# Optimization experiments

Hardware: AMD Instinct MI355X
Metric: run time of the kernel (lower is better)

Reference implementation:

```python
import jax, jax.numpy as jnp
import numpy as np

N = 6144       # nodes
E = 12288      # edges (~2N for a sparse simplicial complex)
NF = 32        # node features
EF = 16        # edge features
NH = [32, 32]  # node_hidden
EH = [16, 16]  # edge_hidden
EPS = 1e-5


def setup_inputs() -> dict:
    key = jax.random.key(0)
    ks = jax.random.split(key, 24)
    s = 0.1  # weight init scale
    inp = {}
    inp["X_n"] = jax.random.normal(ks[0], (N, NF), jnp.float32)
    inp["X_e"] = jax.random.normal(ks[1], (E, EF), jnp.float32)
    # normalized adjacency-like operator (non-negative, row mass ~1)
    inp["A_tilde"] = jax.random.uniform(ks[2], (N, N), jnp.float32) * (1.0 / N)
    # normalized Hodge-1 Laplacian-like operator
    inp["L1_tilde"] = jax.random.normal(ks[3], (E, E), jnp.float32) * (1.0 / np.sqrt(E))
    # incidence-like operator
    inp["B1"] = jax.random.normal(ks[4], (N, E), jnp.float32) * (1.0 / np.sqrt(E))
    # GNN linear layers: weight [out, in] (torch convention)
    inp["gnn_W0"] = jax.random.normal(ks[5], (NH[0], NF), jnp.float32) * s
    inp["gnn_b0"] = jnp.zeros((NH[0],), jnp.float32)
    inp["gnn_W1"] = jax.random.normal(ks[6], (NH[1], NH[0]), jnp.float32) * s
    inp["gnn_b1"] = jnp.zeros((NH[1],), jnp.float32)
    # HoSC layer 0: theta in=EF out=EH[0], BN params
    inp["th_W0"] = jax.random.normal(ks[7], (EH[0], EF), jnp.float32) * s
    inp["th_b0"] = jnp.zeros((EH[0],), jnp.float32)
    inp["bn_g0"] = jnp.ones((EH[0],), jnp.float32)
    inp["bn_b0"] = jnp.zeros((EH[0],), jnp.float32)
    # HoSC layer 1: input collapses to 1 channel (max keepdim)
    inp["th_W1"] = jax.random.normal(ks[8], (EH[1], 1), jnp.float32) * s
    inp["th_b1"] = jnp.zeros((EH[1],), jnp.float32)
    inp["bn_g1"] = jnp.ones((EH[1],), jnp.float32)
    inp["bn_b1"] = jnp.zeros((EH[1],), jnp.float32)
    # head: fc1 in = NH[-1] + len(EH) = 34, out = 2N; fc2 out = 1
    inp["fc1_W"] = jax.random.normal(ks[9], (2 * N, NH[-1] + len(EH)), jnp.float32) * s
    inp["fc1_b"] = jnp.zeros((2 * N,), jnp.float32)
    inp["fc2_W"] = jax.random.normal(ks[10], (1, 2 * N), jnp.float32) * s
    inp["fc2_b"] = jnp.zeros((1,), jnp.float32)
    return inp


def _gnn_layer(A, H, W, b):
    # H <- relu((A @ H) @ W^T + b)
    return jax.nn.relu(jnp.matmul(jnp.matmul(A, H), W.T) + b)


def _hosc_layer(Z, L1, W, b, g, beta):
    Zt = jnp.matmul(Z, W.T) + b            # theta
    Zc = jnp.matmul(L1, Zt)                # Laplacian conv
    m = jnp.mean(Zc, axis=0)               # BatchNorm1d (training-mode batch stats)
    v = jnp.var(Zc, axis=0)
    Zp = jax.nn.relu(g * (Zc - m) * jax.lax.rsqrt(v + EPS) + beta)
    return jnp.max(Zp, axis=1, keepdims=True)  # [E, 1]


def reference(X_n, X_e, A_tilde, L1_tilde, B1,
              gnn_W0, gnn_b0, gnn_W1, gnn_b1,
              th_W0, th_b0, bn_g0, bn_b0,
              th_W1, th_b1, bn_g1, bn_b1,
              fc1_W, fc1_b, fc2_W, fc2_b):
    # GNN over nodes
    H = _gnn_layer(A_tilde, X_n, gnn_W0, gnn_b0)
    H_n = _gnn_layer(A_tilde, H, gnn_W1, gnn_b1)      # [N, NH[-1]]
    # HoSC over edges
    Z0 = _hosc_layer(X_e, L1_tilde, th_W0, th_b0, bn_g0, bn_b0)  # [E, 1]
    Z1 = _hosc_layer(Z0, L1_tilde, th_W1, th_b1, bn_g1, bn_b1)   # [E, 1]
    Z_cat = jnp.concatenate([Z0, Z1], axis=1)         # [E, 2]
    H_e = jnp.matmul(B1, Z_cat)                       # [N, 2]
    # head
    Hcat = jnp.concatenate([H_n, H_e], axis=1)        # [N, 34]
    f = jax.nn.relu(jnp.matmul(Hcat, fc1_W.T) + fc1_b)
    f = jnp.matmul(f, fc2_W.T) + fc2_b                # [N, 1]
    return jax.nn.sigmoid(f).squeeze(-1)              # [N]
```

## Files before the change

### kernel.cpp

```cpp
#include <hip/hip_runtime.h>
#include <hip/hip_bf16.h>
#include <math.h>

#define NND 6144
#define NED 12288
static constexpr float EPS_BN = 1e-5f;

#define HN_OFF    0
#define HE_OFF    196608
#define ST_OFF    208896
#define Y_OFF     208960
#define T0_OFF    405568
#define T1_OFF    602176
#define Z0_OFF    798784
#define Z1_OFF    811072
#define U_OFF     823360
#define S_OFF     835648
#define PP_OFF    847936

typedef float floatx4 __attribute__((ext_vector_type(4)));

__device__ __forceinline__ float4 ntload4(const float* p) {
  floatx4 v = __builtin_nontemporal_load(reinterpret_cast<const floatx4*>(p));
  return make_float4(v.x, v.y, v.z, v.w);
}
__device__ __forceinline__ float4 ld4(const float* p) {
  return *reinterpret_cast<const float4*>(p);
}

__global__ void init_ws(float* __restrict__ p, int n) {
  int i = blockIdx.x * blockDim.x + threadIdx.x;
  if (i < n) p[i] = 0.f;
}

template<int IC, int OC>
__global__ void small_mm_T(const float* __restrict__ X, const float* __restrict__ W,
                           const float* __restrict__ bias, float* __restrict__ CT, int M) {
  int m = blockIdx.x * blockDim.x + threadIdx.x;
  if (m >= M) return;
  float x[IC];
  #pragma unroll
  for (int k = 0; k < IC; k += 4) {
    float4 v = ld4(X + (size_t)m * IC + k);
    x[k] = v.x; x[k+1] = v.y; x[k+2] = v.z; x[k+3] = v.w;
  }
  #pragma unroll
  for (int oc = 0; oc < OC; ++oc) {
    float s = bias ? bias[oc] : 0.f;
    #pragma unroll
    for (int k = 0; k < IC; ++k) s = fmaf(x[k], W[oc * IC + k], s);
    CT[(size_t)oc * M + m] = s;
  }
}

template<int NC, int CG, bool RELU, bool STATS, bool NT>
__global__ __launch_bounds__(256, 3)
void gemm_lds(const float* __restrict__ A, const float* __restrict__ YT,
              const float* __restrict__ bias, float* __restrict__ out,
              float* __restrict__ stats, int K) {
  constexpr int RG = 4 / CG;
  constexpr int ROWS = RG * 4;
  constexpr int SF4 = NC / 4;
  __shared__ float Yb[NC][256];
  __shared__ float sst[32];

  const int tid = threadIdx.x;
  const int lane = tid & 63;
  const int w = tid >> 6;
  const int cg = w % CG, rg = w / CG;
  const int r0 = blockIdx.x * ROWS + rg * 4;
  const int c0 = cg * 16;

  const float* ap[4];
  #pragma unroll
  for (int r = 0; r < 4; ++r) ap[r] = A + (size_t)(r0 + r) * K;

  int srow[SF4], scol[SF4];
  #pragma unroll
  for (int i = 0; i < SF4; ++i) {
    int f = tid + 256 * i;
    srow[i] = f >> 6;
    scol[i] = (f & 63) * 4;
  }

  float4 sreg[SF4], av[4], av2[4];
  float acc[4][16];
  #pragma unroll
  for (int r = 0; r < 4; ++r)
    #pragma unroll
    for (int c = 0; c < 16; ++c) acc[r][c] = 0.f;

  auto stage = [&](int kb) {
    #pragma unroll
    for (int i = 0; i < SF4; ++i)
      sreg[i] = ld4(YT + (size_t)srow[i] * K + kb + scol[i]);
  };
  auto loadA = [&](int kb, float4* dst) {
    #pragma unroll
    for (int r = 0; r < 4; ++r)
      dst[r] = NT ? ntload4(ap[r] + kb + lane * 4) : ld4(ap[r] + kb + lane * 4);
  };

  stage(0);
  loadA(0, av2);

  for (int kb = 0; kb < K; kb += 256) {
    __syncthreads();
    #pragma unroll
    for (int i = 0; i < SF4; ++i)
      *reinterpret_cast<float4*>(&Yb[srow[i]][scol[i]]) = sreg[i];
    #pragma unroll
    for (int r = 0; r < 4; ++r) av[r] = av2[r];
    if (kb + 256 < K) {
      stage(kb + 256);
      loadA(kb + 256, av2);
    }
    __syncthreads();
    #pragma unroll
    for (int c = 0; c < 16; ++c) {
      const float4 y = *reinterpret_cast<const float4*>(&Yb[c0 + c][lane * 4]);
      #pragma unroll
      for (int r = 0; r < 4; ++r) {
        acc[r][c] = fmaf(av[r].x, y.x, acc[r][c]);
        acc[r][c] = fmaf(av[r].y, y.y, acc[r][c]);
        acc[r][c] = fmaf(av[r].z, y.z, acc[r][c]);
        acc[r][c] = fmaf(av[r].w, y.w, acc[r][c]);
      }
    }
  }

  float wv[64];
  #pragma unroll
  for (int r = 0; r < 4; ++r)
    #pragma unroll
    for (int c = 0; c < 16; ++c) wv[r * 16 + c] = acc[r][c];
  #pragma unroll
  for (int b = 5; b >= 0; --b) {
    const int m = 1 << b;
    const bool hi = (lane & m) != 0;
    #pragma unroll
    for (int i = 0; i < (1 << b); ++i) {
      float a  = wv[i];
      float bb = wv[i + (1 << b)];
      float send = hi ? a : bb;
      float recv = __shfl_xor(send, m, 64);
      wv[i] = (hi ? bb : a) + recv;
    }
  }

  const int rsel = lane >> 4, csel = lane & 15;
  float v = wv[0] + (bias ? bias[c0 + csel] : 0.f);
  if (RELU) v = fmaxf(v, 0.f);
  out[(size_t)(r0 + rsel) * NC + c0 + csel] = v;

  if (STATS) {
    if (tid < 32) sst[tid] = 0.f;
    __syncthreads();
    float sv = v, qv = v * v;
    sv += __shfl_xor(sv, 16, 64); sv += __shfl_xor(sv, 32, 64);
    qv += __shfl_xor(qv, 16, 64); qv += __shfl_xor(qv, 32, 64);
    if (lane < 16) { atomicAdd(&sst[csel], sv); atomicAdd(&sst[16 + csel], qv); }
    __syncthreads();
    if (tid < 32) atomicAdd(stats + tid, sst[tid]);
  }
}

template<int MODE>
__global__ __launch_bounds__(256)
void rowpass(const float* __restrict__ Mt, const float* __restrict__ za,
             const float* __restrict__ zb, float* __restrict__ o1,
             float* __restrict__ o2, int K) {
  const int lane = threadIdx.x & 63;
  const int row = blockIdx.x * 4 + (threadIdx.x >> 6);
  const float* mp = Mt + (size_t)row * K;
  float accA = 0.f, accB = 0.f;
  float4 a0 = ntload4(mp + lane * 4);
  float4 a1 = ntload4(mp + 256 + lane * 4);
  for (int kb = 0; kb < K; kb += 512) {
    const int k = kb + lane * 4;
    float4 n0, n1;
    const bool more = (kb + 512) < K;
    if (more) {
      n0 = ntload4(mp + k + 512);
      n1 = ntload4(mp + k + 768);
    }
    float4 z0 = ld4(za + k);
    float4 z1 = ld4(za + k + 256);
    if (MODE == 0) {
      accA += a0.x*z0.x + a0.y*z0.y + a0.z*z0.z + a0.w*z0.w
            + a1.x*z1.x + a1.y*z1.y + a1.z*z1.z + a1.w*z1.w;
      accB += a0.x + a0.y + a0.z + a0.w + a1.x + a1.y + a1.z + a1.w;
    } else {
      float4 y0 = ld4(zb + k);
      float4 y1 = ld4(zb + k + 256);
      accA += a0.x*z0.x + a0.y*z0.y + a0.z*z0.z + a0.w*z0.w
            + a1.x*z1.x + a1.y*z1.y + a1.z*z1.z + a1.w*z1.w;
      accB += a0.x*y0.x + a0.y*y0.y + a0.z*y0.z + a0.w*y0.w
            + a1.x*y1.x + a1.y*y1.y + a1.z*y1.z + a1.w*y1.w;
    }
    if (more) { a0 = n0; a1 = n1; }
  }
  #pragma unroll
  for (int m = 1; m < 64; m <<= 1) {
    accA += __shfl_xor(accA, m, 64);
    accB += __shfl_xor(accB, m, 64);
  }
  if (lane == 0) {
    if (MODE == 0) { o1[row] = accA; o2[row] = accB; }
    else { o1[row * 2] = accA; o1[row * 2 + 1] = accB; }
  }
}

__global__ void bn_max(const float* __restrict__ Zc, const float* __restrict__ stats,
                       const float* __restrict__ g, const float* __restrict__ beta,
                       float* __restrict__ Z, int E) {
  const int e = blockIdx.x * blockDim.x + threadIdx.x;
  if (e >= E) return;
  const float invE = 1.f / (float)E;
  float best = -3.4e38f;
  #pragma unroll
  for (int c = 0; c < 16; ++c) {
    float m = stats[c] * invE;
    float var = stats[16 + c] * invE - m * m;
    float sc = g[c] * rsqrtf(var + EPS_BN);
    float sh = beta[c] - m * sc;
    float x = Zc[(size_t)e * 16 + c];
    best = fmaxf(best, fmaf(x, sc, sh));
  }
  Z[e] = fmaxf(best, 0.f);
}

__global__ void us_stats(const float* __restrict__ u, const float* __restrict__ s,
                         float* __restrict__ st5) {
  const int e = blockIdx.x * 256 + threadIdx.x;
  const int lane = threadIdx.x & 63;
  const int w = threadIdx.x >> 6;
  const float uu = u[e], ss = s[e];
  float v[5] = {uu, ss, uu * uu, ss * ss, uu * ss};
  #pragma unroll
  for (int i = 0; i < 5; ++i)
    #pragma unroll
    for (int m = 1; m < 64; m <<= 1) v[i] += __shfl_xor(v[i], m, 64);
  __shared__ float red[4][5];
  if (lane == 0) {
    #pragma unroll
    for (int i = 0; i < 5; ++i) red[w][i] = v[i];
  }
  __syncthreads();
  if (threadIdx.x < 5) {
    float t = red[0][threadIdx.x] + red[1][threadIdx.x] + red[2][threadIdx.x] + red[3][threadIdx.x];
    atomicAdd(st5 + threadIdx.x, t);
  }
}

__global__ void z1_from_us(const float* __restrict__ u, const float* __restrict__ s,
                           const float* __restrict__ st5,
                           const float* __restrict__ W1, const float* __restrict__ b1,
                           const float* __restrict__ g, const float* __restrict__ beta,
                           float* __restrict__ Z1, int E) {
  const int e = blockIdx.x * blockDim.x + threadIdx.x;
  if (e >= E) return;
  const float invE = 1.f / (float)E;
  const float Su = st5[0], Ss = st5[1], Suu = st5[2], Sss = st5[3], Sus = st5[4];
  const float uu = u[e], ssv = s[e];
  float best = -3.4e38f;
  #pragma unroll
  for (int c = 0; c < 16; ++c) {
    const float wc = W1[c], bc = b1[c];
    const float mean = (wc * Su + bc * Ss) * invE;
    const float ex2 = (wc * wc * Suu + 2.f * wc * bc * Sus + bc * bc * Sss) * invE;
    const float var = ex2 - mean * mean;
    const float sc = g[c] * rsqrtf(var + EPS_BN);
    const float sh = beta[c] - mean * sc;
    best = fmaxf(best, fmaf(wc * uu + bc * ssv, sc, sh));
  }
  Z1[e] = fmaxf(best, 0.f);
}

__global__ __launch_bounds__(256, 2)
void head(const float* __restrict__ Hn, const float* __restrict__ he,
          const float* __restrict__ W1, const float* __restrict__ b1,
          const float* __restrict__ w2, float* __restrict__ prepart) {
  const int t = threadIdx.x;
  const int nb = blockIdx.x;
  const int jb = blockIdx.y;
  int n[3];
  float h[3][34];
  float acc[3] = {0.f, 0.f, 0.f};
  #pragma unroll
  for (int i = 0; i < 3; ++i) {
    n[i] = nb * 768 + i * 256 + t;
    #pragma unroll
    for (int k = 0; k < 32; k += 4) {
      float4 v = ld4(Hn + (size_t)n[i] * 32 + k);
      h[i][k] = v.x; h[i][k+1] = v.y; h[i][k+2] = v.z; h[i][k+3] = v.w;
    }
    float2 e2 = *reinterpret_cast<const float2*>(he + n[i] * 2);
    h[i][32] = e2.x;
    h[i][33] = e2.y;
  }
  const int j0 = jb * 192;
  for (int j = j0; j < j0 + 192; ++j) {
    const float* wp = W1 + (size_t)j * 34;
    const float bj = b1[j], vj = w2[j];
    float s0 = bj, s1 = bj, s2 = bj;
    #pragma unroll
    for (int k = 0; k < 34; ++k) {
      const float wk = wp[k];
      s0 = fmaf(h[0][k], wk, s0);
      s1 = fmaf(h[1][k], wk, s1);
      s2 = fmaf(h[2][k], wk, s2);
    }
    acc[0] += fmaxf(s0, 0.f) * vj;
    acc[1] += fmaxf(s1, 0.f) * vj;
    acc[2] += fmaxf(s2, 0.f) * vj;
  }
  #pragma unroll
  for (int i = 0; i < 3; ++i) prepart[(size_t)jb * NND + n[i]] = acc[i];
}

__global__ void final_k(const float* __restrict__ pp, const float* __restrict__ b2,
                        float* __restrict__ out, int Nn) {
  const int i = blockIdx.x * blockDim.x + threadIdx.x;
  if (i >= Nn) return;
  float s = 0.f;
  #pragma unroll
  for (int j = 0; j < 64; ++j) s += pp[(size_t)j * NND + i];
  out[i] = 1.f / (1.f + expf(-(s + b2[0])));
}

extern "C" void kernel_launch(void* const* d_in, const int* in_sizes, int n_in,
                              void* d_out, int out_size, void* d_ws, size_t ws_size,
                              hipStream_t stream) {
  const float* X_n   = (const float*)d_in[0];
  const float* X_e   = (const float*)d_in[1];
  const float* A     = (const float*)d_in[2];
  const float* L1    = (const float*)d_in[3];
  const float* B1    = (const float*)d_in[4];
  const float* gW0   = (const float*)d_in[5];
  const float* gb0   = (const float*)d_in[6];
  const float* gW1   = (const float*)d_in[7];
  const float* gb1   = (const float*)d_in[8];
  const float* tW0   = (const float*)d_in[9];
  const float* tb0   = (const float*)d_in[10];
  const float* bng0  = (const float*)d_in[11];
  const float* bnb0  = (const float*)d_in[12];
  const float* tW1   = (const float*)d_in[13];
  const float* tb1   = (const float*)d_in[14];
  const float* bng1  = (const float*)d_in[15];
  const float* bnb1  = (const float*)d_in[16];
  const float* fc1W  = (const float*)d_in[17];
  const float* fc1b  = (const float*)d_in[18];
  const float* fc2W  = (const float*)d_in[19];
  const float* fc2b  = (const float*)d_in[20];

  float* ws   = (float*)d_ws;
  float* Hn   = ws + HN_OFF;
  float* he   = ws + HE_OFF;
  float* st   = ws + ST_OFF;
  float* Y    = ws + Y_OFF;
  float* T0   = ws + T0_OFF;
  float* T1   = ws + T1_OFF;
  float* Z0   = ws + Z0_OFF;
  float* Z1   = ws + Z1_OFF;
  float* u    = ws + U_OFF;
  float* s    = ws + S_OFF;
  float* pp   = ws + PP_OFF;
  float* out  = (float*)d_out;

  init_ws<<<1, 64, 0, stream>>>(st, 64);

  small_mm_T<32, 32><<<24, 256, 0, stream>>>(X_n, gW0, nullptr, Y, NND);
  gemm_lds<32, 2, true, false, false><<<768, 256, 0, stream>>>(A, Y, gb0, T0, nullptr, NND);
  small_mm_T<32, 32><<<24, 256, 0, stream>>>(T0, gW1, nullptr, Y, NND);
  gemm_lds<32, 2, true, false, false><<<768, 256, 0, stream>>>(A, Y, gb1, Hn, nullptr, NND);

  small_mm_T<16, 16><<<48, 256, 0, stream>>>(X_e, tW0, tb0, T1, NED);
  gemm_lds<16, 1, false, true, true><<<768, 256, 0, stream>>>(L1, T1, nullptr, T0, st, NED);
  bn_max<<<48, 256, 0, stream>>>(T0, st, bng0, bnb0, Z0, NED);

  rowpass<0><<<3072, 256, 0, stream>>>(L1, Z0, nullptr, u, s, NED);
  us_stats<<<48, 256, 0, stream>>>(u, s, st + 32);
  z1_from_us<<<48, 256, 0, stream>>>(u, s, st + 32, tW1, tb1, bng1, bnb1, Z1, NED);

  rowpass<1><<<1536, 256, 0, stream>>>(B1, Z0, Z1, he, nullptr, NED);

  head<<<dim3(8, 64), 256, 0, stream>>>(Hn, he, fc1W, fc1b, fc2W, pp);
  final_k<<<24, 256, 0, stream>>>(pp, fc2b, out, NND);
}
```

Baseline: 610.5 us.

## Double-buffer GEMM tiles via direct global-to-LDS loads and reverse second L1 pass

```diff
diff --git a/kernel.cpp b/kernel.cpp
--- a/kernel.cpp
+++ b/kernel.cpp
@@ -28,6 +28,12 @@
   return *reinterpret_cast<const float4*>(p);
 }
 
+__device__ __forceinline__ void gll16(const float* g, float* l) {
+  __builtin_amdgcn_global_load_lds(
+      (const __attribute__((address_space(1))) unsigned int*)g,
+      (__attribute__((address_space(3))) unsigned int*)l, 16, 0, 0);
+}
+
 __global__ void init_ws(float* __restrict__ p, int n) {
   int i = blockIdx.x * blockDim.x + threadIdx.x;
   if (i < n) p[i] = 0.f;
@@ -53,72 +59,61 @@
   }
 }
 
-template<int NC, int CG, bool RELU, bool STATS, bool NT>
-__global__ __launch_bounds__(256, 3)
-void gemm_lds(const float* __restrict__ A, const float* __restrict__ YT,
-              const float* __restrict__ bias, float* __restrict__ out,
-              float* __restrict__ stats, int K) {
+template<int NC, int CG, bool RELU, bool STATS>
+__global__ __launch_bounds__(256, 2)
+void gemm_pipe(const float* __restrict__ A, const float* __restrict__ YT,
+               const float* __restrict__ bias, float* __restrict__ out,
+               float* __restrict__ stats, int K) {
   constexpr int RG = 4 / CG;
   constexpr int ROWS = RG * 4;
-  constexpr int SF4 = NC / 4;
-  __shared__ float Yb[NC][256];
+  constexpr int YR_W = NC / 4;
+  constexpr int AR_W = ROWS / 4;
+  constexpr int G = YR_W + AR_W;
+  __shared__ float Yb[2][NC][256];
+  __shared__ float Ab[2][ROWS][256];
   __shared__ float sst[32];
 
   const int tid = threadIdx.x;
   const int lane = tid & 63;
   const int w = tid >> 6;
   const int cg = w % CG, rg = w / CG;
-  const int r0 = blockIdx.x * ROWS + rg * 4;
+  const int r0 = blockIdx.x * ROWS;
   const int c0 = cg * 16;
 
-  const float* ap[4];
-  #pragma unroll
-  for (int r = 0; r < 4; ++r) ap[r] = A + (size_t)(r0 + r) * K;
-
-  int srow[SF4], scol[SF4];
-  #pragma unroll
-  for (int i = 0; i < SF4; ++i) {
-    int f = tid + 256 * i;
-    srow[i] = f >> 6;
-    scol[i] = (f & 63) * 4;
-  }
-
-  float4 sreg[SF4], av[4], av2[4];
+  auto stage = [&](int kb, int b) {
+    #pragma unroll
+    for (int i = 0; i < YR_W; ++i) {
+      const int yr = w * YR_W + i;
+      gll16(YT + (size_t)yr * K + kb + lane * 4, &Yb[b][yr][0]);
+    }
+    #pragma unroll
+    for (int i = 0; i < AR_W; ++i) {
+      const int ar = w * AR_W + i;
+      gll16(A + (size_t)(r0 + ar) * K + kb + lane * 4, &Ab[b][ar][0]);
+    }
+  };
+
   float acc[4][16];
   #pragma unroll
   for (int r = 0; r < 4; ++r)
     #pragma unroll
     for (int c = 0; c < 16; ++c) acc[r][c] = 0.f;
 
-  auto stage = [&](int kb) {
-    #pragma unroll
-    for (int i = 0; i < SF4; ++i)
-      sreg[i] = ld4(YT + (size_t)srow[i] * K + kb + scol[i]);
-  };
-  auto loadA = [&](int kb, float4* dst) {
+  stage(0, 0);
+  stage(256, 1);
+  asm volatile("s_waitcnt vmcnt(%0)" :: "n"(G) : "memory");
+  __builtin_amdgcn_sched_barrier(0);
+  __builtin_amdgcn_s_barrier();
+
+  int cur = 0;
+  for (int kb = 0; kb < K; kb += 256) {
+    float4 av[4];
     #pragma unroll
     for (int r = 0; r < 4; ++r)
-      dst[r] = NT ? ntload4(ap[r] + kb + lane * 4) : ld4(ap[r] + kb + lane * 4);
-  };
-
-  stage(0);
-  loadA(0, av2);
-
-  for (int kb = 0; kb < K; kb += 256) {
-    __syncthreads();
-    #pragma unroll
-    for (int i = 0; i < SF4; ++i)
-      *reinterpret_cast<float4*>(&Yb[srow[i]][scol[i]]) = sreg[i];
-    #pragma unroll
-    for (int r = 0; r < 4; ++r) av[r] = av2[r];
-    if (kb + 256 < K) {
-      stage(kb + 256);
-      loadA(kb + 256, av2);
-    }
-    __syncthreads();
+      av[r] = *reinterpret_cast<const float4*>(&Ab[cur][rg * 4 + r][lane * 4]);
     #pragma unroll
     for (int c = 0; c < 16; ++c) {
-      const float4 y = *reinterpret_cast<const float4*>(&Yb[c0 + c][lane * 4]);
+      const float4 y = *reinterpret_cast<const float4*>(&Yb[cur][c0 + c][lane * 4]);
       #pragma unroll
       for (int r = 0; r < 4; ++r) {
         acc[r][c] = fmaf(av[r].x, y.x, acc[r][c]);
@@ -127,6 +122,16 @@
         acc[r][c] = fmaf(av[r].w, y.w, acc[r][c]);
       }
     }
+    __builtin_amdgcn_s_barrier();
+    if (kb + 512 < K) {
+      stage(kb + 512, cur);
+      asm volatile("s_waitcnt vmcnt(%0)" :: "n"(G) : "memory");
+    } else {
+      asm volatile("s_waitcnt vmcnt(0)" ::: "memory");
+    }
+    __builtin_amdgcn_sched_barrier(0);
+    __builtin_amdgcn_s_barrier();
+    cur ^= 1;
   }
 
   float wv[64];
@@ -149,9 +154,10 @@
   }
 
   const int rsel = lane >> 4, csel = lane & 15;
+  const int rw = rg * 4;
   float v = wv[0] + (bias ? bias[c0 + csel] : 0.f);
   if (RELU) v = fmaxf(v, 0.f);
-  out[(size_t)(r0 + rsel) * NC + c0 + csel] = v;
+  out[(size_t)(r0 + rw + rsel) * NC + c0 + csel] = v;
 
   if (STATS) {
     if (tid < 32) sst[tid] = 0.f;
@@ -165,40 +171,47 @@
   }
 }
 
-template<int MODE>
+template<int MODE, bool REV>
 __global__ __launch_bounds__(256)
 void rowpass(const float* __restrict__ Mt, const float* __restrict__ za,
              const float* __restrict__ zb, float* __restrict__ o1,
              float* __restrict__ o2, int K) {
   const int lane = threadIdx.x & 63;
-  const int row = blockIdx.x * 4 + (threadIdx.x >> 6);
+  const int blk = REV ? (gridDim.x - 1 - blockIdx.x) : blockIdx.x;
+  const int row = blk * 4 + (threadIdx.x >> 6);
   const float* mp = Mt + (size_t)row * K;
   float accA = 0.f, accB = 0.f;
   float4 a0 = ntload4(mp + lane * 4);
   float4 a1 = ntload4(mp + 256 + lane * 4);
+  float4 z0 = ld4(za + lane * 4);
+  float4 z1 = ld4(za + 256 + lane * 4);
+  float4 y0, y1;
+  if (MODE == 1) { y0 = ld4(zb + lane * 4); y1 = ld4(zb + 256 + lane * 4); }
   for (int kb = 0; kb < K; kb += 512) {
     const int k = kb + lane * 4;
-    float4 n0, n1;
     const bool more = (kb + 512) < K;
+    float4 na0, na1, nz0, nz1, ny0, ny1;
     if (more) {
-      n0 = ntload4(mp + k + 512);
-      n1 = ntload4(mp + k + 768);
-    }
-    float4 z0 = ld4(za + k);
-    float4 z1 = ld4(za + k + 256);
+      na0 = ntload4(mp + k + 512);
+      na1 = ntload4(mp + k + 768);
+      nz0 = ld4(za + k + 512);
+      nz1 = ld4(za + k + 768);
+      if (MODE == 1) { ny0 = ld4(zb + k + 512); ny1 = ld4(zb + k + 768); }
+    }
     if (MODE == 0) {
       accA += a0.x*z0.x + a0.y*z0.y + a0.z*z0.z + a0.w*z0.w
             + a1.x*z1.x + a1.y*z1.y + a1.z*z1.z + a1.w*z1.w;
       accB += a0.x + a0.y + a0.z + a0.w + a1.x + a1.y + a1.z + a1.w;
     } else {
-      float4 y0 = ld4(zb + k);
-      float4 y1 = ld4(zb + k + 256);
       accA += a0.x*z0.x + a0.y*z0.y + a0.z*z0.z + a0.w*z0.w
             + a1.x*z1.x + a1.y*z1.y + a1.z*z1.z + a1.w*z1.w;
       accB += a0.x*y0.x + a0.y*y0.y + a0.z*y0.z + a0.w*y0.w
             + a1.x*y1.x + a1.y*y1.y + a1.z*y1.z + a1.w*y1.w;
     }
-    if (more) { a0 = n0; a1 = n1; }
+    if (more) {
+      a0 = na0; a1 = na1; z0 = nz0; z1 = nz1;
+      if (MODE == 1) { y0 = ny0; y1 = ny1; }
+    }
   }
   #pragma unroll
   for (int m = 1; m < 64; m <<= 1) {
@@ -371,19 +384,19 @@
   init_ws<<<1, 64, 0, stream>>>(st, 64);
 
   small_mm_T<32, 32><<<24, 256, 0, stream>>>(X_n, gW0, nullptr, Y, NND);
-  gemm_lds<32, 2, true, false, false><<<768, 256, 0, stream>>>(A, Y, gb0, T0, nullptr, NND);
+  gemm_pipe<32, 2, true, false><<<768, 256, 0, stream>>>(A, Y, gb0, T0, nullptr, NND);
   small_mm_T<32, 32><<<24, 256, 0, stream>>>(T0, gW1, nullptr, Y, NND);
-  gemm_lds<32, 2, true, false, false><<<768, 256, 0, stream>>>(A, Y, gb1, Hn, nullptr, NND);
+  gemm_pipe<32, 2, true, false><<<768, 256, 0, stream>>>(A, Y, gb1, Hn, nullptr, NND);
 
   small_mm_T<16, 16><<<48, 256, 0, stream>>>(X_e, tW0, tb0, T1, NED);
-  gemm_lds<16, 1, false, true, true><<<768, 256, 0, stream>>>(L1, T1, nullptr, T0, st, NED);
+  gemm_pipe<16, 1, false, true><<<768, 256, 0, stream>>>(L1, T1, nullptr, T0, st, NED);
   bn_max<<<48, 256, 0, stream>>>(T0, st, bng0, bnb0, Z0, NED);
 
-  rowpass<0><<<3072, 256, 0, stream>>>(L1, Z0, nullptr, u, s, NED);
+  rowpass<0, true><<<3072, 256, 0, stream>>>(L1, Z0, nullptr, u, s, NED);
   us_stats<<<48, 256, 0, stream>>>(u, s, st + 32);
   z1_from_us<<<48, 256, 0, stream>>>(u, s, st + 32, tW1, tb1, bng1, bnb1, Z1, NED);
 
-  rowpass<1><<<1536, 256, 0, stream>>>(B1, Z0, Z1, he, nullptr, NED);
+  rowpass<1, false><<<1536, 256, 0, stream>>>(B1, Z0, Z1, he, nullptr, NED);
 
   head<<<dim3(8, 64), 256, 0, stream>>>(Hn, he, fc1W, fc1b, fc2W, pp);
   final_k<<<24, 256, 0, stream>>>(pp, fc2b, out, NND);
```

Result: slower. 659.5 us (+8.0%).
